# Kernel optimization log

Hardware: AMD Instinct MI355X
Metric: run time of the kernel (lower is better)

Reference implementation:

```python
import jax, jax.numpy as jnp
import numpy as np

D_MODEL = 2048
SLOTS = 8
D_FIELD = 256  # SLOTS * D_FIELD == proj output dim == 2048
BATCH = 2
SEQ = 4096


def setup_inputs() -> dict:
    key = jax.random.key(0)
    k1, k2 = jax.random.split(key, 2)
    x = jax.random.normal(k1, (BATCH, SEQ, D_MODEL), dtype=jnp.float32)
    # nn.Linear(d_model, slots*d_field): weight [out, in], bias [out]
    W = jax.random.normal(k2, (SLOTS * D_FIELD, D_MODEL), dtype=jnp.float32) * (1.0 / np.sqrt(D_MODEL))
    b = jnp.zeros((SLOTS * D_FIELD,), dtype=jnp.float32)
    horizons = jnp.array([1., 2., 4., 8., 16., 32., 64., 128.], dtype=jnp.float32)
    alphas = jnp.exp(-1.0 / horizons)  # per-slot EMA decay, length SLOTS
    return {"x": x, "W": W, "b": b, "alphas": alphas}


def reference(x, W, b, alphas):
    B, S, _ = x.shape
    # projection: [B,S,d_model] @ [d_model, slots*d_field] -> [B,S,slots,d_field]
    updates = (jnp.einsum('bsd,od->bso', x, W) + b).reshape(B, S, SLOTS, D_FIELD)
    # linear recurrence state_t = alpha * state_{t-1} + u_t, state_0 = 0,
    # via log-depth associative scan with elements (a_t, u_t)
    a = jnp.broadcast_to(alphas[None, None, :, None], updates.shape)

    def combine(c1, c2):
        a1, u1 = c1
        a2, u2 = c2
        return (a1 * a2, a2 * u1 + u2)

    _, state = jax.lax.associative_scan(combine, (a, updates), axis=1)
    return state  # [B,S,slots,d_field]
```

## Files before the change

### kernel.cpp

```cpp
#include <hip/hip_runtime.h>
#include <hip/hip_bf16.h>
#include <stdint.h>
#include <stddef.h>

#define D_MODEL 2048
#define NOUT    2048
#define BATCH   2
#define SEQ     4096
#define M_TOTAL (BATCH*SEQ)
#define SLOTS   8
#define D_FIELD 256
#define CHUNK   32
#define NCHUNK  (SEQ/CHUNK)
#define NT      (D_MODEL/64)

typedef __attribute__((ext_vector_type(4))) float  floatx4;
typedef __attribute__((ext_vector_type(8))) __bf16 bf16x8;
typedef __attribute__((ext_vector_type(4))) __bf16 bf16x4;

__device__ __forceinline__ void async_copy16(const void* gsrc, void* ldst) {
  __builtin_amdgcn_global_load_lds(
      (__attribute__((address_space(1))) const void*)(uintptr_t)gsrc,
      (__attribute__((address_space(3))) void*)(uintptr_t)ldst,
      16, 0, 0);
}

__global__ void cast_kernel(const float* __restrict__ x,
                            const float* __restrict__ W,
                            __bf16* __restrict__ xb,
                            __bf16* __restrict__ wb,
                            int* __restrict__ ctr) {
  if (blockIdx.x == 0 && threadIdx.x < 8)
    __hip_atomic_store(&ctr[threadIdx.x], 0, __ATOMIC_RELAXED, __HIP_MEMORY_SCOPE_AGENT);
  const long long nx = (long long)M_TOTAL * D_MODEL;
  const long long nw = (long long)NOUT * D_MODEL;
  long long base = ((long long)blockIdx.x * blockDim.x + threadIdx.x) * 4;
  if (base < nx) {
    float4 v = *(const float4*)(x + base);
    bf16x4 o;
    o[0] = (__bf16)v.x; o[1] = (__bf16)v.y; o[2] = (__bf16)v.z; o[3] = (__bf16)v.w;
    *(bf16x4*)(xb + base) = o;
  } else {
    long long j = base - nx;
    if (j < nw) {
      float4 v = *(const float4*)(W + j);
      bf16x4 o;
      o[0] = (__bf16)v.x; o[1] = (__bf16)v.y; o[2] = (__bf16)v.z; o[3] = (__bf16)v.w;
      *(bf16x4*)(wb + j) = o;
    }
  }
}

#define VMW4 asm volatile("s_waitcnt vmcnt(4)" ::: "memory")
#define VMW2 asm volatile("s_waitcnt vmcnt(2)" ::: "memory")
#define VMW0 asm volatile("s_waitcnt vmcnt(0)" ::: "memory")
#define LGKM0 do{ asm volatile("s_waitcnt lgkmcnt(0)" ::: "memory"); \
                  __builtin_amdgcn_sched_barrier(0); }while(0)
#define BAR do{ __builtin_amdgcn_s_barrier(); __builtin_amdgcn_sched_barrier(0); }while(0)

#define DSRD(off) (*(const bf16x8*)(smem + (off)))

#define STG(GP, ROFF, DSTOFF, KTN) do{ \
  async_copy16((GP) + (ROFF) + (KTN)*64,      smem + (DSTOFF)); \
  async_copy16((GP) + (ROFF) + (KTN)*64 + 32, smem + (DSTOFF) + 1024); }while(0)

#define RD_AF(BUF, MOFF) do{ \
  _Pragma("unroll") for (int i_ = 0; i_ < 4; ++i_){ \
  _Pragma("unroll") for (int k_ = 0; k_ < 2; ++k_){ \
    afr[i_][k_] = DSRD((BUF)*32768 + ((wM8+(MOFF)+i_)*2+k_)*1024 + fragOff); }} }while(0)

#define RD_BF(BUF, NOFF, DST) do{ \
  _Pragma("unroll") for (int j_ = 0; j_ < 2; ++j_){ \
  _Pragma("unroll") for (int k_ = 0; k_ < 2; ++k_){ \
    DST[j_][k_] = DSRD(65536 + (BUF)*32768 + ((wN4+(NOFF)+j_)*2+k_)*1024 + fragOff); }} }while(0)

#define MFMA_Q(AM, AN, BFR) do{ \
  __builtin_amdgcn_s_setprio(1); \
  _Pragma("unroll") for (int i_ = 0; i_ < 4; ++i_){ \
  _Pragma("unroll") for (int j_ = 0; j_ < 2; ++j_){ \
  _Pragma("unroll") for (int k_ = 0; k_ < 2; ++k_){ \
    acc[(AM)+i_][(AN)+j_] = __builtin_amdgcn_mfma_f32_16x16x32_bf16( \
        afr[i_][k_], BFR[j_][k_], acc[(AM)+i_][(AN)+j_], 0, 0, 0); }}} \
  __builtin_amdgcn_s_setprio(0); }while(0)

#define KTILE(BUF, KTN, DO_STG) do{ \
   \
  RD_AF(BUF, 0); \
  RD_BF(BUF, 0, bfr0); \
  if (DO_STG) STG(gA, rA0, ((BUF)^1)*32768 + dA0, KTN); \
  if (DO_STG) { VMW4; } else { VMW2; } \
  BAR; LGKM0; \
  MFMA_Q(0, 0, bfr0); \
   \
  RD_BF(BUF, 2, bfr1); \
  if (DO_STG) STG(gB, rB0, ((BUF)^1)*32768 + dB0, KTN); \
  if (DO_STG) { VMW4; } else { VMW0; } \
  BAR; LGKM0; \
  MFMA_Q(0, 2, bfr1); \
   \
  RD_AF(BUF, 4); \
  if (DO_STG) STG(gB, rB1, ((BUF)^1)*32768 + dB1, KTN); \
  BAR; LGKM0; \
  MFMA_Q(4, 2, bfr1); \
   \
  if (DO_STG) { STG(gA, rA1, ((BUF)^1)*32768 + dA1, KTN); VMW4; } \
  BAR; \
  MFMA_Q(4, 0, bfr0); \
}while(0)

#define CARRY_LD(P) __hip_atomic_load((P), __ATOMIC_RELAXED, __HIP_MEMORY_SCOPE_AGENT)

__global__ __launch_bounds__(512, 2) void gemm_scan_kernel(
    const __bf16* __restrict__ A,
    const __bf16* __restrict__ Bw,
    const float*  __restrict__ bias,
    const float*  __restrict__ alphas,
    float* __restrict__ C,
    float* __restrict__ carry,
    int*   __restrict__ ctr) {
  extern __shared__ __align__(16) char smem[];
  const int t    = threadIdx.x;
  const int lane = t & 63;
  const int w    = t >> 6;
  const int wM   = w >> 2;
  const int wN   = w & 3;
  const int m0   = blockIdx.x * 256;
  const int n0   = blockIdx.y * 256;

  const int lq = lane >> 4, lr = lane & 15;
  const int fragOff = (lr*64 + lq*16) ^ (((lr >> 3) & 1) << 5);
  const int wM8 = wM*8, wN4 = wN*4;

  const int lrow = lane >> 2;
  const int lcol = ((lane & 3) * 8) ^ ((lane >> 5) * 16);
  const int srA0 = (w & 3) + ((w >> 2) << 3), srA1 = srA0 + 4;
  const int srB0 = (w & 1) + ((w >> 1) << 2), srB1 = srB0 + 2;
  const __bf16* gA = A  + (size_t)m0 * D_MODEL + lcol;
  const __bf16* gB = Bw + (size_t)n0 * D_MODEL + lcol;
  const int rA0 = (srA0*16 + lrow) * D_MODEL;
  const int rA1 = (srA1*16 + lrow) * D_MODEL;
  const int rB0 = (srB0*16 + lrow) * D_MODEL;
  const int rB1 = (srB1*16 + lrow) * D_MODEL;
  const int dA0 = srA0*2048 + lane*16;
  const int dA1 = srA1*2048 + lane*16;
  const int dB0 = 65536 + srB0*2048 + lane*16;
  const int dB1 = 65536 + srB1*2048 + lane*16;

  floatx4 acc[8][4] = {};
  bf16x8 afr[4][2], bfr0[2][2], bfr1[2][2];

  STG(gA, rA0, dA0, 0);
  STG(gB, rB0, dB0, 0);
  STG(gB, rB1, dB1, 0);
  STG(gA, rA1, dA1, 0);
  VMW4;
  BAR;

#pragma unroll 1
  for (int p = 0; p < 15; ++p) {
    KTILE(0, 2*p+1, true);
    KTILE(1, 2*p+2, true);
  }
  KTILE(0, 31, true);
  KTILE(1, 0, false);

  const int mW0 = m0 + wM*128;
  const int nW0 = n0 + wN*64;
  const float alpha = alphas[nW0 >> 8];
  const float a2 = alpha*alpha, a4 = a2*a2, a8 = a4*a4, a16 = a8*a8, a32 = a16*a16;
  float aq = 1.f;
#pragma unroll
  for (int i = 0; i < 3; ++i) if (i < 3 - lq) aq *= a4;
  float a4p = 1.f;
#pragma unroll
  for (int i = 0; i < 3; ++i) if (i < lq) a4p *= a4;
  const int bb  = mW0 >> 12;
  const int j0w = (mW0 & (SEQ - 1)) >> 5;
  float* cbase = carry + (size_t)bb * NCHUNK * NOUT;

  float bvv[4], tmv[4][8];
#pragma unroll
  for (int nf = 0; nf < 4; ++nf) {
    const int n = nW0 + nf*16 + lr;
    bvv[nf] = bias[n];
    const float bv = bvv[nf];
#pragma unroll
    for (int mf = 0; mf < 8; ++mf) {
      const floatx4 av = acc[mf][nf];
      tmv[nf][mf] = (((av[0]+bv)*alpha + (av[1]+bv))*alpha + (av[2]+bv))*alpha + (av[3]+bv);
    }
#pragma unroll
    for (int c = 0; c < 4; ++c) {
      float s = (tmv[nf][2*c]*a16 + tmv[nf][2*c+1]) * aq;
      s += __shfl_xor(s, 16, 64);
      s += __shfl_xor(s, 32, 64);
      if (lq == 0)
        __hip_atomic_store(&cbase[(size_t)(j0w + c)*NOUT + n], s,
                           __ATOMIC_RELAXED, __HIP_MEMORY_SCOPE_AGENT);
    }
  }

  __syncthreads();
  if (t == 0) {
    __hip_atomic_fetch_add(&ctr[blockIdx.y], 1, __ATOMIC_ACQ_REL, __HIP_MEMORY_SCOPE_AGENT);
    while (__hip_atomic_load(&ctr[blockIdx.y], __ATOMIC_ACQUIRE, __HIP_MEMORY_SCOPE_AGENT) < 32)
      __builtin_amdgcn_s_sleep(2);
  }
  __syncthreads();

  {
    const float* cbl = cbase + (nW0 + lq*16 + lr);
    float H = 0.f;
#pragma unroll 4
    for (int jp = 0; jp < j0w; ++jp)
      H = a32*H + CARRY_LD(&cbl[(size_t)jp*NOUT]);
    float s0[4];
#pragma unroll
    for (int nf = 0; nf < 4; ++nf) s0[nf] = __shfl(H, nf*16 + lr, 64);

#pragma unroll
    for (int nf = 0; nf < 4; ++nf) {
      const int n = nW0 + nf*16 + lr;
      const float bv = bvv[nf];
      float sp = s0[nf];
#pragma unroll
      for (int c = 0; c < 4; ++c) {
        if (c > 0)
          sp = a32*sp + CARRY_LD(&cbase[(size_t)(j0w + c - 1)*NOUT + n]);
        float ulo[4], uhi[4];
#pragma unroll
        for (int i = 0; i < 4; ++i) {
          ulo[i] = acc[2*c][nf][i]   + bv;
          uhi[i] = acc[2*c+1][nf][i] + bv;
        }
        const float Tlo = tmv[nf][2*c];
        const float Thi = tmv[nf][2*c+1];
        const float t0  = __shfl(Tlo, lr,      64);
        const float t1  = __shfl(Tlo, 16 + lr, 64);
        const float t2  = __shfl(Tlo, 32 + lr, 64);
        const float t3  = __shfl(Tlo, 48 + lr, 64);
        const float th0 = __shfl(Thi, lr,      64);
        const float th1 = __shfl(Thi, 16 + lr, 64);
        const float th2 = __shfl(Thi, 32 + lr, 64);
        float h = 0.f;
        if (lq > 0) h = t0;
        if (lq > 1) h = h*a4 + t1;
        if (lq > 2) h = h*a4 + t2;
        float Slo = a4p*sp + h;
        const float smid = (((t0*a4 + t1)*a4 + t2)*a4 + t3) + a16*sp;
        float hh = 0.f;
        if (lq > 0) hh = th0;
        if (lq > 1) hh = hh*a4 + th1;
        if (lq > 2) hh = hh*a4 + th2;
        float Shi = a4p*smid + hh;
        const size_t rowb = (size_t)(mW0 + 2*c*16 + lq*4);
        float s = Slo;
#pragma unroll
        for (int i = 0; i < 4; ++i) { s = alpha*s + ulo[i]; C[(rowb + i)*NOUT + n] = s; }
        s = Shi;
#pragma unroll
        for (int i = 0; i < 4; ++i) { s = alpha*s + uhi[i]; C[(rowb + 16 + i)*NOUT + n] = s; }
      }
    }
  }
}

extern "C" void kernel_launch(void* const* d_in, const int* in_sizes, int n_in,
                              void* d_out, int out_size, void* d_ws, size_t ws_size,
                              hipStream_t stream) {
  const float* x      = (const float*)d_in[0];
  const float* W      = (const float*)d_in[1];
  const float* bias   = (const float*)d_in[2];
  const float* alphas = (const float*)d_in[3];
  float* out = (float*)d_out;

  __bf16* xb   = (__bf16*)d_ws;
  __bf16* wb   = (__bf16*)((char*)d_ws + (size_t)M_TOTAL * D_MODEL * 2);
  float* carry = (float*)((char*)d_ws + (size_t)M_TOTAL * D_MODEL * 2
                                       + (size_t)NOUT * D_MODEL * 2);
  int* ctr     = (int*)((char*)d_ws + (size_t)M_TOTAL * D_MODEL * 2
                                     + (size_t)NOUT * D_MODEL * 2
                                     + (size_t)BATCH * NCHUNK * NOUT * 4);

  {
    const long long total = ((long long)M_TOTAL * D_MODEL + (long long)NOUT * D_MODEL) / 4;
    const int blocks = (int)((total + 255) / 256);
    cast_kernel<<<blocks, 256, 0, stream>>>(x, W, xb, wb, ctr);
  }
  {
    dim3 grid(M_TOTAL / 256, NOUT / 256);
    gemm_scan_kernel<<<grid, 512, 131072, stream>>>(xb, wb, bias, alphas, out, carry, ctr);
  }
}
```

Before: 208.4 us.

## Aggregate chunk carries per wave and batch carry loads in prefix scan

Each wave now folds its four 32-row chunk carries into a single 128-row carry before publishing it, which cuts global carry traffic by four. The local chunk carries stay in registers for the intra-wave prefix instead of being reloaded from global memory. The cross-wave prefix loop issues eight independent loads per iteration and combines them with precomputed alpha powers, shortening the serial dependent-load chain. The cost is extra registers and more powers of alpha, which slightly changes floating-point rounding.

```diff
diff --git a/kernel.cpp b/kernel.cpp
--- a/kernel.cpp
+++ b/kernel.cpp
@@ -12,7 +12,7 @@
 #define D_FIELD 256
 #define CHUNK   32
 #define NCHUNK  (SEQ/CHUNK)
-#define NT      (D_MODEL/64)
+#define NWAVEC  64
 
 typedef __attribute__((ext_vector_type(4))) float  floatx4;
 typedef __attribute__((ext_vector_type(8))) __bf16 bf16x8;
@@ -116,7 +116,7 @@
     const float*  __restrict__ bias,
     const float*  __restrict__ alphas,
     float* __restrict__ C,
-    float* __restrict__ carry,
+    float* __restrict__ wc,
     int*   __restrict__ ctr) {
   extern __shared__ __align__(16) char smem[];
   const int t    = threadIdx.x;
@@ -168,6 +168,8 @@
   const int nW0 = n0 + wN*64;
   const float alpha = alphas[nW0 >> 8];
   const float a2 = alpha*alpha, a4 = a2*a2, a8 = a4*a4, a16 = a8*a8, a32 = a16*a16;
+  const float a64 = a32*a32, a128 = a64*a64;
+  const float a256 = a128*a128, a512 = a256*a256, a1024 = a512*a512;
   float aq = 1.f;
 #pragma unroll
   for (int i = 0; i < 3; ++i) if (i < 3 - lq) aq *= a4;
@@ -176,9 +178,10 @@
   for (int i = 0; i < 3; ++i) if (i < lq) a4p *= a4;
   const int bb  = mW0 >> 12;
   const int j0w = (mW0 & (SEQ - 1)) >> 5;
-  float* cbase = carry + (size_t)bb * NCHUNK * NOUT;
-
-  float bvv[4], tmv[4][8];
+  const int jw  = j0w >> 2;
+  float* wcb = wc + (size_t)bb * NWAVEC * NOUT;
+
+  float bvv[4], tmv[4][8], rcl[4][4];
 #pragma unroll
   for (int nf = 0; nf < 4; ++nf) {
     const int n = nW0 + nf*16 + lr;
@@ -194,10 +197,12 @@
       float s = (tmv[nf][2*c]*a16 + tmv[nf][2*c+1]) * aq;
       s += __shfl_xor(s, 16, 64);
       s += __shfl_xor(s, 32, 64);
-      if (lq == 0)
-        __hip_atomic_store(&cbase[(size_t)(j0w + c)*NOUT + n], s,
-                           __ATOMIC_RELAXED, __HIP_MEMORY_SCOPE_AGENT);
-    }
+      rcl[nf][c] = s;
+    }
+    const float Wv = ((rcl[nf][0]*a32 + rcl[nf][1])*a32 + rcl[nf][2])*a32 + rcl[nf][3];
+    if (lq == 0)
+      __hip_atomic_store(&wcb[(size_t)jw*NOUT + n], Wv,
+                         __ATOMIC_RELAXED, __HIP_MEMORY_SCOPE_AGENT);
   }
 
   __syncthreads();
@@ -209,11 +214,22 @@
   __syncthreads();
 
   {
-    const float* cbl = cbase + (nW0 + lq*16 + lr);
+    const float* wcl = wcb + (nW0 + lq*16 + lr);
     float H = 0.f;
-#pragma unroll 4
-    for (int jp = 0; jp < j0w; ++jp)
-      H = a32*H + CARRY_LD(&cbl[(size_t)jp*NOUT]);
+    int jp = 0;
+    for (; jp + 8 <= jw; jp += 8) {
+      float v[8];
+#pragma unroll
+      for (int i = 0; i < 8; ++i)
+        v[i] = CARRY_LD(&wcl[(size_t)(jp + i)*NOUT]);
+      float h = v[0];
+#pragma unroll
+      for (int i = 1; i < 8; ++i) h = h*a128 + v[i];
+      H = H*a1024 + h;
+    }
+    for (; jp < jw; ++jp)
+      H = H*a128 + CARRY_LD(&wcl[(size_t)jp*NOUT]);
+
     float s0[4];
 #pragma unroll
     for (int nf = 0; nf < 4; ++nf) s0[nf] = __shfl(H, nf*16 + lr, 64);
@@ -226,7 +242,7 @@
 #pragma unroll
       for (int c = 0; c < 4; ++c) {
         if (c > 0)
-          sp = a32*sp + CARRY_LD(&cbase[(size_t)(j0w + c - 1)*NOUT + n]);
+          sp = a32*sp + rcl[nf][c-1];
         float ulo[4], uhi[4];
 #pragma unroll
         for (int i = 0; i < 4; ++i) {
@@ -274,13 +290,13 @@
   const float* alphas = (const float*)d_in[3];
   float* out = (float*)d_out;
 
-  __bf16* xb   = (__bf16*)d_ws;
-  __bf16* wb   = (__bf16*)((char*)d_ws + (size_t)M_TOTAL * D_MODEL * 2);
-  float* carry = (float*)((char*)d_ws + (size_t)M_TOTAL * D_MODEL * 2
-                                       + (size_t)NOUT * D_MODEL * 2);
-  int* ctr     = (int*)((char*)d_ws + (size_t)M_TOTAL * D_MODEL * 2
-                                     + (size_t)NOUT * D_MODEL * 2
-                                     + (size_t)BATCH * NCHUNK * NOUT * 4);
+  __bf16* xb = (__bf16*)d_ws;
+  __bf16* wb = (__bf16*)((char*)d_ws + (size_t)M_TOTAL * D_MODEL * 2);
+  float* wc  = (float*)((char*)d_ws + (size_t)M_TOTAL * D_MODEL * 2
+                                     + (size_t)NOUT * D_MODEL * 2);
+  int* ctr   = (int*)((char*)d_ws + (size_t)M_TOTAL * D_MODEL * 2
+                                   + (size_t)NOUT * D_MODEL * 2
+                                   + (size_t)BATCH * NWAVEC * NOUT * 4);
 
   {
     const long long total = ((long long)M_TOTAL * D_MODEL + (long long)NOUT * D_MODEL) / 4;
@@ -289,6 +305,6 @@
   }
   {
     dim3 grid(M_TOTAL / 256, NOUT / 256);
-    gemm_scan_kernel<<<grid, 512, 131072, stream>>>(xb, wb, bias, alphas, out, carry, ctr);
+    gemm_scan_kernel<<<grid, 512, 131072, stream>>>(xb, wb, bias, alphas, out, wc, ctr);
   }
 }
```

After: 199.0 us. 4.5% less time.
